# Performance work log

Measured on AMD Instinct MI355X. Metric: run time of the kernel, lower is better.

The kernel has to match this reference:

```python
import math
import numpy as np
import jax, jax.numpy as jnp

# ---- static configuration (matches init_kwargs) ----
B_IN, B_OUT = 32, 16            # bandwidths: input grid 64^3, output grid 32^3
F_IN, F_OUT, BATCH = 16, 32, 8
_ALPHAS = np.arange(8) * (np.pi / 4.0)
_BETAS = (np.arange(3) + 1.0) * (np.pi / 24.0)
GRID = np.array([[a, b, 0.0] for b in _BETAS for a in _ALPHAS])
NGRID = GRID.shape[0]
SCALING = 1.0 / math.sqrt(NGRID * F_IN * B_OUT ** 3 / B_IN ** 3)


def _wigner_d(l, beta):
    # Wigner small-d matrix d^l_{m'm}(beta); quantum normalization, centered
    # order (m', m in -l..l), Condon-Shortley phase. Log-factorials for stability.
    lf = np.zeros(2 * l + 1)
    if l > 0:
        lf[1:] = np.cumsum(np.log(np.arange(1, 2 * l + 1, dtype=np.float64)))
    cb, sb = np.cos(beta / 2.0), np.sin(beta / 2.0)
    d = np.zeros((2 * l + 1, 2 * l + 1))
    for i, mp in enumerate(range(-l, l + 1)):
        for j, m in enumerate(range(-l, l + 1)):
            pref = 0.5 * (lf[l + mp] + lf[l - mp] + lf[l + m] + lf[l - m])
            acc = 0.0
            for s in range(max(0, m - mp), min(l + m, l - mp) + 1):
                logden = lf[l + m - s] + lf[s] + lf[mp - m + s] + lf[l - mp - s]
                acc += ((-1.0) ** (mp - m + s)) * np.exp(pref - logden) \
                       * cb ** (2 * l + m - mp - 2 * s) * sb ** (mp - m + 2 * s)
            d[i, j] = acc
    return d


def _dh_weights(b):
    # Driscoll-Healy / SOFT quadrature weights for sin(beta) d(beta) on 2b betas.
    j = np.arange(2 * b)
    k = np.arange(b)
    return (2.0 / b) * np.sin(np.pi * (2 * j + 1) / (4.0 * b)) * (
        np.sin(np.pi * np.outer(2 * j + 1, 2 * k + 1) / (4.0 * b)) @ (1.0 / (2 * k + 1)))


# ---- precomputed Wigner transform matrices (numpy, setup-time only) ----
_betas_in = (np.arange(2 * B_IN) + 0.5) * np.pi / (2 * B_IN)
_betas_out = (np.arange(2 * B_OUT) + 0.5) * np.pi / (2 * B_OUT)
_w = _dh_weights(B_IN)
WIG_FWD, WIG_INV, D_GRID = [], [], []
for l in range(B_OUT):
    dji = np.stack([_wigner_d(l, bt) for bt in _betas_in])   # [2b_in, 2l+1, 2l+1]
    WIG_FWD.append((dji * _w[:, None, None] / (2.0 * (2 * B_IN) ** 2)).astype(np.float32))
    djo = np.stack([_wigner_d(l, bt) for bt in _betas_out])  # [2b_out, 2l+1, 2l+1]
    WIG_INV.append(((2 * l + 1) * djo).astype(np.float32))
    m = np.arange(-l, l + 1)
    dg = np.stack([_wigner_d(l, g) for g in GRID[:, 1]])     # [G, 2l+1, 2l+1]
    D = np.exp(-1j * np.outer(GRID[:, 0], m))[:, :, None] * dg \
        * np.exp(-1j * np.outer(GRID[:, 2], m))[:, None, :]  # full Wigner D on grid
    D_GRID.append(D.astype(np.complex64))


def setup_inputs():
    key = jax.random.key(0)
    k1, k2 = jax.random.split(key)
    x = jax.random.normal(k1, (BATCH, F_IN, 2 * B_IN, 2 * B_IN, 2 * B_IN), dtype=jnp.float32)
    kernel = jax.random.uniform(k2, (F_IN, F_OUT, NGRID), dtype=jnp.float32, minval=-1.0, maxval=1.0)
    bias = jnp.zeros((1, F_OUT, 1, 1, 1), dtype=jnp.float32)
    return {"x": x, "kernel": kernel, "bias": bias}


def reference(x, kernel, bias):
    # x: [batch, f_in, beta, alpha, gamma] on the 2b_in SOFT grid.
    N_in, N_out = 2 * B_IN, 2 * B_OUT
    # SO(3) FFT stage 1: plain FFT over (alpha, gamma).
    xf = jnp.fft.fft2(x.astype(jnp.complex64), axes=(-2, -1))  # [B, F_in, beta, m, n]
    ker = (kernel * SCALING).astype(jnp.complex64)
    S = jnp.zeros((x.shape[0], F_OUT, N_out, N_out, N_out), dtype=jnp.complex64)
    for l in range(B_OUT):  # irregular, order-dependent spectral blocks
        idx = np.arange(-l, l + 1) % N_in  # centered frequencies -l..l (wrapped)
        xx = xf[:, :, :, idx[:, None], idx[None, :]]                      # [B,F_in,2b_in,2l+1,2l+1]
        Fx = jnp.einsum('jmn,bfjmn->bfmn', jnp.asarray(WIG_FWD[l]), xx)   # weighted Wigner-d over beta
        Fy = jnp.einsum('gmn,iog->iomn', jnp.asarray(D_GRID[l]), ker)     # so3_rft of kernel
        Fz = jnp.einsum('bimk,ionk->bomn', Fx, jnp.conj(Fy))              # so3_mm: Fz^l = Fx^l (Fy^l)^H
        contrib = jnp.einsum('jmn,bomn->bojmn', jnp.asarray(WIG_INV[l]), Fz)
        odx = np.arange(-l, l + 1) % N_out
        S = S.at[:, :, :, odx[:, None], odx[None, :]].add(contrib)
    out = jnp.fft.ifft2(S, axes=(-2, -1)).real * float(N_out * N_out)     # inverse SO(3) FFT (real)
    return out + bias
```

## Files before the change

### kernel.cpp

```cpp
#include <hip/hip_runtime.h>
#include <math.h>

#define NIN   64
#define NOUT  32
#define NL    16
#define NFIN  16
#define NFOUT 32
#define NB    8
#define NGRID 24
#define NFREQ 31
#define TOTL  5456
#define NTAB  540144

#define WF_F   0
#define WI_F   349184
#define DGC_F  523776
#define W64_F  785664
#define W32_F  789632
#define XFS_F  791616
#define FX_F   16536640
#define FYC_F  17933376
#define FZ_F   23520320

#define FZ_ELEMS 1396736
#define NJOBS 1680
#define CNT_OFF (XFS_F + 3 * 2 * FZ_ELEMS)

__device__ __forceinline__ int offl(int l) { return l * (2 * l - 1) * (2 * l + 1) / 3; }

__device__ __forceinline__ double ipow(double x, int n) {
    double r = 1.0, p = x;
    while (n) { if (n & 1) r *= p; p *= p; n >>= 1; }
    return r;
}

__device__ const int JOB_START[17] = {0, 256, 496, 720, 928, 1072, 1204, 1324, 1432,
                                      1496, 1552, 1600, 1640, 1656, 1668, 1676, 1680};

__global__ __launch_bounds__(256) void k_tables(float* __restrict__ WF, float* __restrict__ WI,
                                                float2* __restrict__ DGC, float2* __restrict__ W64,
                                                float2* __restrict__ W32) {
    __shared__ double lfs[32];
    __shared__ double wdh[64];
    const double PI = 3.14159265358979323846264338327950288;
    int tid = threadIdx.x;
    if (tid < 32) {
        double f = 1.0;
        for (int i = 2; i <= tid; ++i) f *= (double)i;
        lfs[tid] = log(f);
    } else if (tid < 96) {
        int j = tid - 32;
        double x1 = PI * (double)(2 * j + 1) / 128.0;
        double ssum = 0.0;
        for (int k = 0; k < 32; ++k) ssum += sin(x1 * (double)(2 * k + 1)) / (double)(2 * k + 1);
        wdh[j] = (2.0 / 32.0) * sin(x1) * ssum;
    }
    __syncthreads();

    int t = blockIdx.x * 256 + tid;
    if (t >= NTAB) {
        int u = t - NTAB;
        if (u < 31 * 64) {
            int f = u >> 6, p = u & 63;
            double ang = -2.0 * PI * (double)((f - 15) * p) / 64.0;
            W64[u] = make_float2((float)cos(ang), (float)sin(ang));
        } else {
            u -= 31 * 64;
            if (u < 31 * 32) {
                int mu = u >> 5, p = u & 31;
                double ang = 2.0 * PI * (double)((mu - 15) * p) / 32.0;
                W32[u] = make_float2((float)cos(ang), (float)sin(ang));
            }
        }
        return;
    }
    int l = 0;
    while (l < 15 && t >= 99 * offl(l + 1)) l++;
    int n1 = 2 * l + 1, n2 = n1 * n1;
    int r = t - 99 * offl(l);
    int src = r / n2;
    int e = r - src * n2;
    int a = e / n1;
    int b = e - a * n1;
    int mp = a - l, m = b - l;

    double beta;
    if (src < 64)      beta = ((double)src + 0.5) * PI / 64.0;
    else if (src < 96) beta = ((double)(src - 64) + 0.5) * PI / 32.0;
    else               beta = (double)(src - 96 + 1) * PI / 24.0;

    double cb = cos(0.5 * beta), sb = sin(0.5 * beta);
    int smin = (m - mp) > 0 ? (m - mp) : 0;
    int smax = (l + m) < (l - mp) ? (l + m) : (l - mp);
    double pref = 0.5 * (lfs[l + mp] + lfs[l - mp] + lfs[l + m] + lfs[l - m]);
    double logden = lfs[l + m - smin] + lfs[smin] + lfs[mp - m + smin] + lfs[l - mp - smin];
    int p1 = 2 * l + m - mp - 2 * smin;
    int p2 = mp - m + 2 * smin;
    double term = exp(pref - logden) * ipow(cb, p1) * ipow(sb, p2);
    if ((mp - m + smin) & 1) term = -term;
    double acc = term;
    double rr = (sb * sb) / (cb * cb);
    for (int s = smin; s < smax; ++s) {
        term *= -rr * (double)((l + m - s) * (l - mp - s)) / (double)((s + 1) * (mp - m + s + 1));
        acc += term;
    }

    if (src < 64) {
        int j = src;
        WF[64 * offl(l) + (j * n1 + a) * n1 + b] = (float)(acc * wdh[j] / 8192.0);
    } else if (src < 96) {
        int j = src - 64;
        WI[32 * offl(l) + (j * n1 + a) * n1 + b] = (float)((double)(2 * l + 1) * acc);
    } else {
        int bi = src - 96;
        const double SCALING = 0.14433756729740644112728719512549;
        double sc = acc * SCALING;
        int base = 24 * offl(l) + a * n1 + b;
        for (int ai = 0; ai < 8; ++ai) {
            double ang = (double)ai * (PI / 4.0) * (double)(a - l);
            DGC[base + (bi * 8 + ai) * n2] = make_float2((float)(sc * cos(ang)), (float)(sc * sin(ang)));
        }
    }
}

__global__ __launch_bounds__(256) void k_dft2(const float* __restrict__ x, const float2* __restrict__ W64,
                                              float2* __restrict__ XFS) {
    __shared__ float  xs[64 * 64];
    __shared__ float2 a1[64 * 16];
    __shared__ float2 w64s[31 * 65];
    int tid = threadIdx.x;
    int slice = blockIdx.x;
    const float* xp = x + (size_t)slice * 4096;
    for (int i = tid; i < 1024; i += 256) ((float4*)xs)[i] = ((const float4*)xp)[i];
    for (int i = tid; i < 31 * 64; i += 256) { int f = i >> 6, p = i & 63; w64s[f * 65 + p] = W64[i]; }
    __syncthreads();
    for (int o = tid; o < 64 * 16; o += 256) {
        int p = o >> 4, n = o & 15;
        const float* xrow = xs + p * 64;
        const float2* wrow = &w64s[(n + 15) * 65];
        float re = 0.f, im = 0.f;
#pragma unroll 8
        for (int q = 0; q < 64; ++q) { float xv = xrow[q]; float2 w = wrow[q]; re += xv * w.x; im += xv * w.y; }
        a1[p * 16 + n] = make_float2(re, im);
    }
    __syncthreads();
    float2* outp = XFS + (size_t)slice * 961;
    for (int o = tid; o < 31 * 16; o += 256) {
        int mu = o >> 4, n = o & 15;
        const float2* wrow = &w64s[mu * 65];
        float re = 0.f, im = 0.f;
#pragma unroll 8
        for (int p = 0; p < 64; ++p) {
            float2 av = a1[p * 16 + n]; float2 w = wrow[p];
            re += av.x * w.x - av.y * w.y;
            im += av.x * w.y + av.y * w.x;
        }
        outp[mu * 31 + (15 + n)] = make_float2(re, im);
        outp[(30 - mu) * 31 + (15 - n)] = make_float2(re, -im);
    }
}

__global__ __launch_bounds__(256) void k_fy(const float* __restrict__ ker, const float2* __restrict__ DGC,
                                            float2* __restrict__ FYC) {
    int t = blockIdx.x * 256 + threadIdx.x;
    if (t >= 512 * TOTL) return;
    int l = 0;
    while (l < 15 && t >= 512 * offl(l + 1)) l++;
    int n1 = 2 * l + 1, n2 = n1 * n1;
    int r = t - 512 * offl(l);
    int k = r % n1; r /= n1;
    int i = r & 15; r >>= 4;
    int n = r % n1; int o = r / n1;
    const float2* dg = DGC + 24 * offl(l) + n * n1 + k;
    const float* kp = ker + (i * 32 + o) * 24;
    float re = 0.f, im = 0.f;
#pragma unroll
    for (int g = 0; g < 24; ++g) {
        float2 d = dg[g * n2];
        float kv = kp[g];
        re += d.x * kv; im += d.y * kv;
    }
    FYC[t] = make_float2(re, im);
}

__global__ __launch_bounds__(256) void k_fx(const float2* __restrict__ XFS, const float* __restrict__ WF,
                                            float2* __restrict__ FX) {
    int t = blockIdx.x * 256 + threadIdx.x;
    if (t >= 128 * TOTL) return;
    int l = 0;
    while (l < 15 && t >= 128 * offl(l + 1)) l++;
    int n1 = 2 * l + 1, n2 = n1 * n1;
    int r = t - 128 * offl(l);
    int k = r % n1; r /= n1;
    int i = r & 15; r >>= 4;
    int m = r % n1; int b = r / n1;
    const float* wf = WF + 64 * offl(l) + m * n1 + k;
    const float2* xf = XFS + (size_t)((b * 16 + i) * 64) * 961 + (m - l + 15) * 31 + (k - l + 15);
    float re = 0.f, im = 0.f;
#pragma unroll 8
    for (int j = 0; j < 64; ++j) {
        float w = wf[j * n2];
        float2 v = xf[j * 961];
        re += w * v.x; im += w * v.y;
    }
    FX[t] = make_float2(re, im);
}

__global__ __launch_bounds__(256) void k_fz(const float2* __restrict__ FX, const float2* __restrict__ FYC,
                                            float2* __restrict__ P0, float2* __restrict__ P1,
                                            float2* __restrict__ P2, float2* __restrict__ P3,
                                            int* __restrict__ cnt) {
    __shared__ float2 As[2][64][17];
    __shared__ float2 Bs[2][64][17];
    __shared__ int sjob;
    int tid = threadIdx.x;
    int kk0 = tid & 15;
    int rr0 = tid >> 4;
    int ty = tid >> 4;
    int tx = tid & 15;

    for (;;) {
        if (tid == 0) sjob = atomicAdd(cnt, 1);
        __syncthreads();
        int bid = sjob;
        if (bid >= NJOBS) return;

        int li = 0;
        while (li < 15 && bid >= JOB_START[li + 1]) ++li;
        int l = 15 - li;
        int n1 = 2 * l + 1;
        int ntn = (n1 + 1) >> 1;
        int r = bid - JOB_START[li];
        int ic = r & 3; r >>= 2;
        int tn = r % ntn;
        int tm = r / ntn;
        int M = 8 * n1, N = 32 * n1, K = 16 * n1;
        int kend = 4 * n1;
        int cbase = ic * kend;
        const float2* A = FX + 128 * offl(l);
        const float2* B = FYC + 512 * offl(l);
        float2* C = (ic == 0 ? P0 : ic == 1 ? P1 : ic == 2 ? P2 : P3) + 256 * offl(l);

        float acr[4][4] = {{0}}, aci[4][4] = {{0}};
        float2 ar[4], br[4];
        {
            int kc = kk0;
            bool kok = kc < kend;
#pragma unroll
            for (int s = 0; s < 4; ++s) {
                int row = rr0 + 16 * s;
                int grow = tm * 64 + row;
                ar[s] = (kok && grow < M) ? A[(size_t)grow * K + cbase + kc] : make_float2(0.f, 0.f);
                int gcol = tn * 64 + row;
                br[s] = (kok && gcol < N) ? B[(size_t)gcol * K + cbase + kc] : make_float2(0.f, 0.f);
            }
        }
        int cur = 0;
        for (int k0 = 0; k0 < kend; k0 += 16) {
#pragma unroll
            for (int s = 0; s < 4; ++s) {
                As[cur][rr0 + 16 * s][kk0] = ar[s];
                Bs[cur][rr0 + 16 * s][kk0] = br[s];
            }
            __syncthreads();
            if (k0 + 16 < kend) {
                int kc = k0 + 16 + kk0;
                bool kok = kc < kend;
#pragma unroll
                for (int s = 0; s < 4; ++s) {
                    int row = rr0 + 16 * s;
                    int grow = tm * 64 + row;
                    ar[s] = (kok && grow < M) ? A[(size_t)grow * K + cbase + kc] : make_float2(0.f, 0.f);
                    int gcol = tn * 64 + row;
                    br[s] = (kok && gcol < N) ? B[(size_t)gcol * K + cbase + kc] : make_float2(0.f, 0.f);
                }
            }
#pragma unroll
            for (int kk = 0; kk < 16; ++kk) {
                float2 av[4], bv[4];
#pragma unroll
                for (int ii = 0; ii < 4; ++ii) av[ii] = As[cur][ty + 16 * ii][kk];
#pragma unroll
                for (int jj = 0; jj < 4; ++jj) bv[jj] = Bs[cur][tx + 16 * jj][kk];
#pragma unroll
                for (int ii = 0; ii < 4; ++ii)
#pragma unroll
                    for (int jj = 0; jj < 4; ++jj) {
                        acr[ii][jj] += av[ii].x * bv[jj].x - av[ii].y * bv[jj].y;
                        aci[ii][jj] += av[ii].x * bv[jj].y + av[ii].y * bv[jj].x;
                    }
            }
            cur ^= 1;
        }
#pragma unroll
        for (int ii = 0; ii < 4; ++ii) {
            int row = tm * 64 + ty + 16 * ii;
            if (row >= M) continue;
#pragma unroll
            for (int jj = 0; jj < 4; ++jj) {
                int col = tn * 64 + tx + 16 * jj;
                if (col < N) C[(size_t)row * N + col] = make_float2(acr[ii][jj], aci[ii][jj]);
            }
        }
        __syncthreads();
    }
}

__global__ __launch_bounds__(256) void k_reduce(float4* __restrict__ FZ, const float4* __restrict__ P1,
                                                const float4* __restrict__ P2, const float4* __restrict__ P3) {
    int t = blockIdx.x * 256 + threadIdx.x;
    if (t >= FZ_ELEMS / 2) return;
    float4 a = FZ[t], b = P1[t], c = P2[t], d = P3[t];
    a.x += b.x + c.x + d.x;
    a.y += b.y + c.y + d.y;
    a.z += b.z + c.z + d.z;
    a.w += b.w + c.w + d.w;
    FZ[t] = a;
}

__global__ __launch_bounds__(256) void k_out(const float2* __restrict__ FZ, const float* __restrict__ WI,
                                             const float2* __restrict__ W32, const float* __restrict__ bias,
                                             float* __restrict__ out) {
    __shared__ float2 s31[961];
    __shared__ float2 w32s[31 * 33];
    __shared__ float2 T[31 * 32];
    int tid = threadIdx.x;
    int slice = blockIdx.x;
    int j = slice & 31;
    int o = (slice >> 5) & 31;
    int b = slice >> 10;
    for (int i = tid; i < 992; i += 256) { int mu = i >> 5, p = i & 31; w32s[mu * 33 + p] = W32[i]; }
    for (int t = tid; t < 961; t += 256) {
        int mu = t / 31;
        int nu = t - mu * 31;
        int m = mu - 15, n = nu - 15;
        int am = m < 0 ? -m : m, an = n < 0 ? -n : n;
        int l0 = am > an ? am : an;
        float re = 0.f, im = 0.f;
        for (int l = l0; l < 16; ++l) {
            int n1 = 2 * l + 1;
            int off = offl(l);
            float w = WI[32 * off + (j * n1 + (m + l)) * n1 + (n + l)];
            float2 z = FZ[256 * off + (size_t)(b * n1 + (m + l)) * (32 * n1) + o * n1 + (n + l)];
            re += w * z.x; im += w * z.y;
        }
        s31[t] = make_float2(re, im);
    }
    __syncthreads();
    for (int t = tid; t < 992; t += 256) {
        int mu = t >> 5, q = t & 31;
        const float2* srow = s31 + mu * 31;
        float re = 0.f, im = 0.f;
#pragma unroll
        for (int nu = 0; nu < 31; ++nu) {
            float2 sv = srow[nu]; float2 w = w32s[nu * 33 + q];
            re += sv.x * w.x - sv.y * w.y;
            im += sv.x * w.y + sv.y * w.x;
        }
        T[mu * 32 + q] = make_float2(re, im);
    }
    __syncthreads();
    float bv = bias[o];
    float* op = out + (size_t)slice * 1024;
    for (int t = tid; t < 1024; t += 256) {
        int p = t >> 5, q = t & 31;
        float acc = 0.f;
#pragma unroll
        for (int mu = 0; mu < 31; ++mu) {
            float2 tv = T[mu * 32 + q]; float2 w = w32s[mu * 33 + p];
            acc += tv.x * w.x - tv.y * w.y;
        }
        op[t] = acc + bv;
    }
}

extern "C" void kernel_launch(void* const* d_in, const int* in_sizes, int n_in,
                              void* d_out, int out_size, void* d_ws, size_t ws_size,
                              hipStream_t stream) {
    const float* x    = (const float*)d_in[0];
    const float* ker  = (const float*)d_in[1];
    const float* bias = (const float*)d_in[2];
    float* out = (float*)d_out;
    float* wsf = (float*)d_ws;

    float*  WF   = wsf + WF_F;
    float*  WI   = wsf + WI_F;
    float2* DGC  = (float2*)(wsf + DGC_F);
    float2* W64  = (float2*)(wsf + W64_F);
    float2* W32  = (float2*)(wsf + W32_F);
    float2* XFS  = (float2*)(wsf + XFS_F);
    float2* FX   = (float2*)(wsf + FX_F);
    float2* FYC  = (float2*)(wsf + FYC_F);
    float2* FZ   = (float2*)(wsf + FZ_F);
    float2* FZP1 = XFS;
    float2* FZP2 = FZP1 + FZ_ELEMS;
    float2* FZP3 = FZP2 + FZ_ELEMS;
    int*    CNT  = (int*)(wsf + CNT_OFF);

    hipLaunchKernelGGL(k_tables, dim3(2122),  dim3(256), 0, stream, WF, WI, DGC, W64, W32);
    hipLaunchKernelGGL(k_dft2,   dim3(8192),  dim3(256), 0, stream, x, W64, XFS);
    hipLaunchKernelGGL(k_fy,     dim3(10912), dim3(256), 0, stream, ker, DGC, FYC);
    hipLaunchKernelGGL(k_fx,     dim3(2728),  dim3(256), 0, stream, XFS, WF, FX);
    hipMemsetAsync(CNT, 0, sizeof(int), stream);
    hipLaunchKernelGGL(k_fz,     dim3(1024),  dim3(256), 0, stream, FX, FYC, FZ, FZP1, FZP2, FZP3, CNT);
    hipLaunchKernelGGL(k_reduce, dim3(2728),  dim3(256), 0, stream, (float4*)FZ, (const float4*)FZP1,
                                                                   (const float4*)FZP2, (const float4*)FZP3);
    hipLaunchKernelGGL(k_out,    dim3(8192),  dim3(256), 0, stream, FZ, WI, W32, bias, out);
}
```

Before: 860.8 us.

## Exploit DFT even/odd symmetry in forward and inverse 2D DFT kernels

```diff
diff --git a/kernel.cpp b/kernel.cpp
--- a/kernel.cpp
+++ b/kernel.cpp
@@ -125,38 +125,80 @@
 
 __global__ __launch_bounds__(256) void k_dft2(const float* __restrict__ x, const float2* __restrict__ W64,
                                               float2* __restrict__ XFS) {
-    __shared__ float  xs[64 * 64];
+    __shared__ float  xs[64 * 65];
     __shared__ float2 a1[64 * 16];
     __shared__ float2 w64s[31 * 65];
     int tid = threadIdx.x;
     int slice = blockIdx.x;
     const float* xp = x + (size_t)slice * 4096;
-    for (int i = tid; i < 1024; i += 256) ((float4*)xs)[i] = ((const float4*)xp)[i];
+    for (int i = tid; i < 1024; i += 256) {
+        float4 v = ((const float4*)xp)[i];
+        int p = i >> 4, q0 = (i & 15) * 4;
+        float* dst = xs + p * 65 + q0;
+        dst[0] = v.x; dst[1] = v.y; dst[2] = v.z; dst[3] = v.w;
+    }
     for (int i = tid; i < 31 * 64; i += 256) { int f = i >> 6, p = i & 63; w64s[f * 65 + p] = W64[i]; }
     __syncthreads();
-    for (int o = tid; o < 64 * 16; o += 256) {
-        int p = o >> 4, n = o & 15;
-        const float* xrow = xs + p * 64;
-        const float2* wrow = &w64s[(n + 15) * 65];
-        float re = 0.f, im = 0.f;
-#pragma unroll 8
-        for (int q = 0; q < 64; ++q) { float xv = xrow[q]; float2 w = wrow[q]; re += xv * w.x; im += xv * w.y; }
-        a1[p * 16 + n] = make_float2(re, im);
+    for (int t = tid; t < 64 * 31; t += 256) {
+        int p = t / 31, q = t - p * 31 + 1;
+        float a = xs[p * 65 + q], b = xs[p * 65 + 64 - q];
+        xs[p * 65 + q] = a + b;
+        xs[p * 65 + 64 - q] = a - b;
+    }
+    __syncthreads();
+    {
+        int n = tid & 15;
+        int prow = tid >> 4;
+        float2 wreg[31];
+#pragma unroll
+        for (int q = 1; q <= 31; ++q) wreg[q - 1] = w64s[(n + 15) * 65 + q];
+        float sg = (n & 1) ? -1.f : 1.f;
+        for (int t2 = 0; t2 < 4; ++t2) {
+            int p = prow + 16 * t2;
+            const float* row = xs + p * 65;
+            float re = row[0] + sg * row[32];
+            float im = 0.f;
+#pragma unroll
+            for (int q = 1; q <= 31; ++q) {
+                re += row[q] * wreg[q - 1].x;
+                im += row[64 - q] * wreg[q - 1].y;
+            }
+            a1[p * 16 + n] = make_float2(re, im);
+        }
+    }
+    __syncthreads();
+    for (int t = tid; t < 31 * 16; t += 256) {
+        int p = (t >> 4) + 1, n = t & 15;
+        float2 a = a1[p * 16 + n], b = a1[(64 - p) * 16 + n];
+        a1[p * 16 + n] = make_float2(a.x + b.x, a.y + b.y);
+        a1[(64 - p) * 16 + n] = make_float2(a.x - b.x, a.y - b.y);
     }
     __syncthreads();
     float2* outp = XFS + (size_t)slice * 961;
-    for (int o = tid; o < 31 * 16; o += 256) {
-        int mu = o >> 4, n = o & 15;
-        const float2* wrow = &w64s[mu * 65];
-        float re = 0.f, im = 0.f;
-#pragma unroll 8
-        for (int p = 0; p < 64; ++p) {
-            float2 av = a1[p * 16 + n]; float2 w = wrow[p];
-            re += av.x * w.x - av.y * w.y;
-            im += av.x * w.y + av.y * w.x;
-        }
-        outp[mu * 31 + (15 + n)] = make_float2(re, im);
-        outp[(30 - mu) * 31 + (15 - n)] = make_float2(re, -im);
+    {
+        int n = tid & 15;
+        int mrow = tid >> 4;
+        for (int t2 = 0; t2 < 2; ++t2) {
+            int mu = mrow + 16 * t2;
+            if (mu >= 31) continue;
+            int f = mu - 15;
+            float sg = (f & 1) ? -1.f : 1.f;
+            float2 A0 = a1[n], A32 = a1[32 * 16 + n];
+            float re = A0.x + sg * A32.x;
+            float im = A0.y + sg * A32.y;
+            const float2* wrow = &w64s[mu * 65];
+#pragma unroll
+            for (int p = 1; p <= 31; ++p) {
+                float2 EA = a1[p * 16 + n];
+                float2 OA = a1[(64 - p) * 16 + n];
+                float c = wrow[p].x;
+                float s = -wrow[p].y;
+                re += EA.x * c + OA.y * s;
+                im += EA.y * c - OA.x * s;
+            }
+            outp[mu * 31 + (15 + n)] = make_float2(re, im);
+            outp[(30 - mu) * 31 + (15 - n)] = make_float2(re, -im);
+        }
     }
 }
 
@@ -323,13 +365,25 @@
                                              float* __restrict__ out) {
     __shared__ float2 s31[961];
     __shared__ float2 w32s[31 * 33];
-    __shared__ float2 T[31 * 32];
+    __shared__ float4 eoB[31 * 15];
+    __shared__ float2 Tb[31 * 32];
+    __shared__ float2 Tc[15 * 32];
+    __shared__ float  T0r[32];
+    __shared__ int    wbase[16], zbase[16], n1v[16], n32v[16];
     int tid = threadIdx.x;
     int slice = blockIdx.x;
     int j = slice & 31;
     int o = (slice >> 5) & 31;
     int b = slice >> 10;
+    if (tid < 16) {
+        int l = tid, n1 = 2 * l + 1;
+        int off = offl(l);
+        wbase[l] = 32 * off + j * n1 * n1;
+        zbase[l] = 256 * off + b * 32 * n1 * n1 + o * n1;
+        n1v[l] = n1; n32v[l] = 32 * n1;
+    }
     for (int i = tid; i < 992; i += 256) { int mu = i >> 5, p = i & 31; w32s[mu * 33 + p] = W32[i]; }
+    __syncthreads();
     for (int t = tid; t < 961; t += 256) {
         int mu = t / 31;
         int nu = t - mu * 31;
@@ -338,39 +392,69 @@
         int l0 = am > an ? am : an;
         float re = 0.f, im = 0.f;
         for (int l = l0; l < 16; ++l) {
-            int n1 = 2 * l + 1;
-            int off = offl(l);
-            float w = WI[32 * off + (j * n1 + (m + l)) * n1 + (n + l)];
-            float2 z = FZ[256 * off + (size_t)(b * n1 + (m + l)) * (32 * n1) + o * n1 + (n + l)];
+            int mi = m + l, ni = n + l;
+            float w = WI[wbase[l] + mi * n1v[l] + ni];
+            float2 z = FZ[zbase[l] + mi * n32v[l] + ni];
             re += w * z.x; im += w * z.y;
         }
         s31[t] = make_float2(re, im);
     }
     __syncthreads();
-    for (int t = tid; t < 992; t += 256) {
-        int mu = t >> 5, q = t & 31;
-        const float2* srow = s31 + mu * 31;
-        float re = 0.f, im = 0.f;
-#pragma unroll
-        for (int nu = 0; nu < 31; ++nu) {
-            float2 sv = srow[nu]; float2 w = w32s[nu * 33 + q];
-            re += sv.x * w.x - sv.y * w.y;
-            im += sv.x * w.y + sv.y * w.x;
-        }
-        T[mu * 32 + q] = make_float2(re, im);
+    for (int t = tid; t < 465; t += 256) {
+        int mu = t / 15, v = t - mu * 15 + 1;
+        float2 a = s31[mu * 31 + 15 + v];
+        float2 c = s31[mu * 31 + 15 - v];
+        eoB[t] = make_float4(a.x + c.x, a.y + c.y, a.x - c.x, a.y - c.y);
+    }
+    __syncthreads();
+    {
+        int q = tid & 31, mg = tid >> 5;
+        float2 wreg[15];
+#pragma unroll
+        for (int v = 1; v <= 15; ++v) wreg[v - 1] = w32s[(v + 15) * 33 + q];
+        for (int t2 = 0; t2 < 4; ++t2) {
+            int mu = mg + 8 * t2;
+            if (mu < 31) {
+                float2 c0 = s31[mu * 31 + 15];
+                float tr = c0.x, ti = c0.y;
+                const float4* ep = &eoB[mu * 15];
+#pragma unroll
+                for (int v = 0; v < 15; ++v) {
+                    float4 e = ep[v];
+                    float c = wreg[v].x, s = wreg[v].y;
+                    tr += e.x * c - e.w * s;
+                    ti += e.y * c + e.z * s;
+                }
+                Tb[mu * 32 + q] = make_float2(tr, ti);
+            }
+        }
+    }
+    __syncthreads();
+    for (int t = tid; t < 512; t += 256) {
+        int v = t >> 5, q = t & 31;
+        if (v == 0) T0r[q] = Tb[15 * 32 + q].x;
+        else {
+            float2 a = Tb[(15 + v) * 32 + q];
+            float2 c = Tb[(15 - v) * 32 + q];
+            Tc[(v - 1) * 32 + q] = make_float2(a.x + c.x, a.y - c.y);
+        }
     }
     __syncthreads();
     float bv = bias[o];
     float* op = out + (size_t)slice * 1024;
-    for (int t = tid; t < 1024; t += 256) {
-        int p = t >> 5, q = t & 31;
-        float acc = 0.f;
-#pragma unroll
-        for (int mu = 0; mu < 31; ++mu) {
-            float2 tv = T[mu * 32 + q]; float2 w = w32s[mu * 33 + p];
-            acc += tv.x * w.x - tv.y * w.y;
-        }
-        op[t] = acc + bv;
+    {
+        int q = tid & 31, pg = tid >> 5;
+        for (int t2 = 0; t2 < 4; ++t2) {
+            int p = pg + 8 * t2;
+            float acc = T0r[q];
+#pragma unroll
+            for (int v = 1; v <= 15; ++v) {
+                float2 tc = Tc[(v - 1) * 32 + q];
+                float2 w = w32s[(v + 15) * 33 + p];
+                acc += tc.x * w.x - tc.y * w.y;
+            }
+            op[p * 32 + q] = acc + bv;
+        }
     }
 }
 
```

Result: faster. 807.3 us (-6.2%).
